# Kernel optimization log

Hardware: AMD Instinct MI355X
Metric: run time of the kernel (lower is better)

The kernel has to match this reference:

```python
import jax, jax.numpy as jnp
import numpy as np

N_NODES = 20000
N_EDGES = 640000
NODE_NF = 64
HIDDEN = 256
N_LAYERS = 4


def _linear_init(key, fan_in, fan_out, layers=None):
    shape = (fan_in, fan_out) if layers is None else (layers, fan_in, fan_out)
    scale = 1.0 / np.sqrt(fan_in)
    return jax.random.normal(key, shape, dtype=jnp.float32) * scale


def setup_inputs() -> dict:
    key = jax.random.key(0)
    ks = jax.random.split(key, 16)
    L, H = N_LAYERS, HIDDEN
    return {
        "h": jax.random.normal(ks[0], (N_NODES, NODE_NF), dtype=jnp.float32),
        "edge_index": jax.random.randint(ks[1], (2, N_EDGES), 0, N_NODES, dtype=jnp.int64),
        "coord_diff": jax.random.normal(ks[2], (N_EDGES, 3), dtype=jnp.float32),
        # embedding in / out
        "w_in": _linear_init(ks[3], NODE_NF, H),
        "b_in": jnp.zeros((H,), jnp.float32),
        "w_out": _linear_init(ks[4], H, NODE_NF),
        "b_out": jnp.zeros((NODE_NF,), jnp.float32),
        # per-layer edge MLP: Linear(2H+1 -> H), silu, Linear(H -> H), silu
        "edge_w1": _linear_init(ks[5], 2 * H + 1, H, L),
        "edge_b1": jnp.zeros((L, H), jnp.float32),
        "edge_w2": _linear_init(ks[6], H, H, L),
        "edge_b2": jnp.zeros((L, H), jnp.float32),
        # per-layer node MLP: Linear(2H -> H), silu, Linear(H -> H)
        "node_w1": _linear_init(ks[7], 2 * H, H, L),
        "node_b1": jnp.zeros((L, H), jnp.float32),
        "node_w2": _linear_init(ks[8], H, H, L),
        "node_b2": jnp.zeros((L, H), jnp.float32),
    }


def reference(h, edge_index, coord_diff, w_in, b_in, w_out, b_out,
              edge_w1, edge_b1, edge_w2, edge_b2,
              node_w1, node_b1, node_w2, node_b2):
    row, col = edge_index[0], edge_index[1]
    # radial is layer-independent: [E, 1]
    radial = jnp.sum(coord_diff ** 2, axis=1, keepdims=True)

    h = h @ w_in + b_in  # [N, H]
    n_nodes = h.shape[0]

    for l in range(N_LAYERS):
        # edge model: gather endpoints, concat with radial, 2-layer MLP
        m = jnp.concatenate([h[row], h[col], radial], axis=1)  # [E, 2H+1]
        m = jax.nn.silu(m @ edge_w1[l] + edge_b1[l])
        m = jax.nn.silu(m @ edge_w2[l] + edge_b2[l])  # [E, H]
        # node model: segment-sum aggregate over row, concat, 2-layer MLP
        agg = jax.ops.segment_sum(m, row, num_segments=n_nodes)  # [N, H]
        x = jnp.concatenate([h, agg], axis=1)  # [N, 2H]
        x = jax.nn.silu(x @ node_w1[l] + node_b1[l])
        h = x @ node_w2[l] + node_b2[l]  # recurrent=False: no residual

    return h @ w_out + b_out  # [N, node_nf]
```

## Files before the change

### kernel.cpp

```cpp
#include <hip/hip_runtime.h>
#include <hip/hip_bf16.h>
#include <cstdint>
#include <cstddef>

#define NN 20000
#define NE 640000
#define NF 64
#define HD 256
#define NL 4
#define HTS 640

typedef __attribute__((ext_vector_type(8))) short short8;
typedef __attribute__((ext_vector_type(4))) float f32x4;
typedef __attribute__((ext_vector_type(2))) float f32x2;

__device__ __forceinline__ float bf2f(unsigned short u){
  union { unsigned int i; float f; } x; x.i = ((unsigned int)u) << 16; return x.f;
}
__device__ __forceinline__ unsigned short f2bf(float f){
  union { float f; unsigned int i; } x; x.f = f;
  unsigned int r = x.i + 0x7FFFu + ((x.i >> 16) & 1u);
  return (unsigned short)(r >> 16);
}
__device__ __forceinline__ unsigned int pk2bf(float a, float b){
  union { __hip_bfloat162 h; unsigned int u; } cv;
  cv.h = __float22bfloat162_rn(float2{a, b});
  return cv.u;
}
__device__ __forceinline__ float silu_f(float v){
  float e = __builtin_amdgcn_exp2f(v * -1.442695041f);
  return v * __builtin_amdgcn_rcpf(1.0f + e);
}
__device__ __forceinline__ f32x2 silu2(f32x2 v){
  f32x2 t = v * (f32x2){-1.442695041f, -1.442695041f};
  f32x2 e = (f32x2){__builtin_amdgcn_exp2f(t.x), __builtin_amdgcn_exp2f(t.y)};
  f32x2 d = e + (f32x2){1.0f, 1.0f};
  f32x2 r = (f32x2){__builtin_amdgcn_rcpf(d.x), __builtin_amdgcn_rcpf(d.y)};
  return v * r;
}
__device__ __forceinline__ void async16(const void* g, void* l){
  __builtin_amdgcn_global_load_lds(
      (const __attribute__((address_space(1))) unsigned int*)g,
      (__attribute__((address_space(3))) unsigned int*)l, 16, 0, 0);
}

__global__ __launch_bounds__(256) void prep_small(
    const float* __restrict__ w_in, const float* __restrict__ w_out,
    const float* __restrict__ ew1, const float* __restrict__ ew2,
    const float* __restrict__ nw1, const float* __restrict__ nw2,
    const float* __restrict__ eb1,
    unsigned short* __restrict__ w_in_t, unsigned short* __restrict__ w_out_t,
    unsigned short* __restrict__ ew1cat, float* __restrict__ w1r,
    float* __restrict__ b1e,
    unsigned short* __restrict__ ew2t, unsigned short* __restrict__ nw1t,
    unsigned short* __restrict__ nw2t)
{
  const int s = blockIdx.y;
  const int tid = blockIdx.x * 256 + threadIdx.x;
  if (s == 18) {
    if (tid < NL * 512) {
      int l = tid >> 9, c = tid & 511;
      b1e[tid] = (c < 256) ? eb1[l * HD + c] : 0.0f;
    }
    return;
  }
  if (s >= 2 && s < 6) {
    int l = s - 2;
    if (tid >= 513 * HD) return;
    int k = tid / HD, n = tid - k * HD;
    float v = ew1[(size_t)l * 513 * HD + tid];
    if (k == 512) { w1r[l * HD + n] = v; return; }
    unsigned short* dst = ew1cat + (size_t)l * 512 * 256;
    if (k < 256) dst[(size_t)n * 256 + k] = f2bf(v);
    else         dst[(size_t)(256 + n) * 256 + (k - 256)] = f2bf(v);
    return;
  }
  const float* src; unsigned short* dst; int K, N;
  if (s == 0)      { src = w_in;  dst = w_in_t;  K = NF;   N = HD; }
  else if (s == 1) { src = w_out; dst = w_out_t; K = HD;   N = NF; }
  else if (s < 10) { int l = s-6;  src = ew2 + (size_t)l*HD*HD;   dst = ew2t + (size_t)l*HD*HD;  K = HD;   N = HD; }
  else if (s < 14) { int l = s-10; src = nw1 + (size_t)l*2*HD*HD; dst = nw1t + (size_t)l*HD*512; K = 2*HD; N = HD; }
  else             { int l = s-14; src = nw2 + (size_t)l*HD*HD;   dst = nw2t + (size_t)l*HD*HD;  K = HD;   N = HD; }
  if (tid >= K * N) return;
  int k = tid / N, n = tid - k * N;
  dst[(size_t)n * K + k] = f2bf(src[tid]);
}

__global__ __launch_bounds__(256) void prep_big(
    const float* __restrict__ h_in, const float* __restrict__ cd,
    unsigned short* __restrict__ hb_in, float* __restrict__ radial)
{
  const int s = blockIdx.y;
  const int tid = blockIdx.x * 256 + threadIdx.x;
  if (s == 0) {
    if (tid < NN * NF) hb_in[tid] = f2bf(h_in[tid]);
  } else {
    if (tid < NE) {
      float x = cd[tid*3+0], y = cd[tid*3+1], z = cd[tid*3+2];
      radial[tid] = x*x + y*y + z*z;
    }
  }
}

__global__ __launch_bounds__(256) void hist_k(const int* __restrict__ erow, int* __restrict__ hist){
  int e = blockIdx.x * 256 + threadIdx.x;
  if (e < NE){
    unsigned r = (unsigned)erow[e]; if (r >= NN) r = 0;
    atomicAdd(&hist[r], 1);
  }
}

__global__ __launch_bounds__(256) void scan_k(const int* __restrict__ hist,
                                              int* __restrict__ starts, int* __restrict__ cursor){
  __shared__ int part[256];
  const int t = threadIdx.x;
  const int CH = 79;
  int lo = t * CH, hi = lo + CH; if (hi > NN) hi = NN; if (lo > NN) lo = NN;
  int s = 0;
  for (int i = lo; i < hi; ++i) s += hist[i];
  part[t] = s; __syncthreads();
  for (int off = 1; off < 256; off <<= 1){
    int v = (t >= off) ? part[t - off] : 0;
    __syncthreads();
    part[t] += v;
    __syncthreads();
  }
  int base = (t == 0) ? 0 : part[t - 1];
  for (int i = lo; i < hi; ++i){ starts[i] = base; cursor[i] = base; base += hist[i]; }
  if (t == 255) starts[NN] = part[255];
}

__global__ __launch_bounds__(256) void scatter_k(const int* __restrict__ erow,
                                                 const int* __restrict__ ecol,
                                                 const float* __restrict__ radial,
                                                 int* __restrict__ cursor,
                                                 int* __restrict__ rowcol,
                                                 float* __restrict__ radial_s){
  int e = blockIdx.x * 256 + threadIdx.x;
  if (e < NE){
    unsigned r = (unsigned)erow[e]; if (r >= NN) r = 0;
    unsigned c = (unsigned)ecol[e]; if (c >= NN) c = 0;
    int pos = atomicAdd(&cursor[r], 1);
    rowcol[2*pos]   = (int)r;
    rowcol[2*pos+1] = (int)c;
    radial_s[pos] = radial[e];
  }
}

__global__ __launch_bounds__(256) void gemm_k(
    const unsigned short* __restrict__ Am, const unsigned short* __restrict__ Wt,
    const float* __restrict__ bias,
    unsigned short* __restrict__ outB, float* __restrict__ outF,
    int M, int N, int K, int lda, int ldc, int fuseSilu)
{
  __shared__ __align__(16) unsigned short As[128*32];
  __shared__ __align__(16) unsigned short Bs[128*32];
  const int t = threadIdx.x;
  const int lane = t & 63, wave = t >> 6;
  const int ln15 = lane & 15, q = lane >> 4;
  const int bm = blockIdx.x, bn = blockIdx.y;
  const int wm = wave >> 1, wn = wave & 1;

  f32x4 acc[4][4];
  #pragma unroll
  for (int i = 0; i < 4; ++i)
    #pragma unroll
    for (int j = 0; j < 4; ++j) acc[i][j] = (f32x4){0.f,0.f,0.f,0.f};

  const int sr = t >> 2;
  const int sc = (t & 3) * 8;
  int am0 = bm*128 + sr;      if (am0 > M-1) am0 = M-1;
  int am1 = bm*128 + 64 + sr; if (am1 > M-1) am1 = M-1;
  int an0 = bn*128 + sr;      if (an0 > N-1) an0 = N-1;
  int an1 = bn*128 + 64 + sr; if (an1 > N-1) an1 = N-1;
  const unsigned short* a0 = Am + (size_t)am0 * lda + sc;
  const unsigned short* a1 = Am + (size_t)am1 * lda + sc;
  const unsigned short* b0 = Wt + (size_t)an0 * K + sc;
  const unsigned short* b1 = Wt + (size_t)an1 * K + sc;

  const int nkt = K >> 5;
  for (int kt = 0; kt < nkt; ++kt) {
    const int k0 = kt * 32;
    async16(a0 + k0, &As[t*8]);
    async16(a1 + k0, &As[2048 + t*8]);
    async16(b0 + k0, &Bs[t*8]);
    async16(b1 + k0, &Bs[2048 + t*8]);
    __syncthreads();
    short8 fa[4], fb[4];
    #pragma unroll
    for (int i = 0; i < 4; ++i)
      fa[i] = *(const short8*)&As[(wm*64 + i*16 + ln15)*32 + q*8];
    #pragma unroll
    for (int j = 0; j < 4; ++j)
      fb[j] = *(const short8*)&Bs[(wn*64 + j*16 + ln15)*32 + q*8];
    #pragma unroll
    for (int i = 0; i < 4; ++i)
      #pragma unroll
      for (int j = 0; j < 4; ++j)
        acc[i][j] = __builtin_amdgcn_mfma_f32_16x16x32_bf16(fa[i], fb[j], acc[i][j], 0, 0, 0);
    __syncthreads();
  }

  #pragma unroll
  for (int i = 0; i < 4; ++i) {
    #pragma unroll
    for (int j = 0; j < 4; ++j) {
      const int n = bn*128 + wn*64 + j*16 + ln15;
      if (n >= N) continue;
      const float bv = bias ? bias[n] : 0.0f;
      #pragma unroll
      for (int r = 0; r < 4; ++r) {
        const int m = bm*128 + wm*64 + i*16 + q*4 + r;
        if (m >= M) continue;
        float v = acc[i][j][r] + bv;
        if (fuseSilu) v = silu_f(v);
        if (outB) outB[(size_t)m * ldc + n] = f2bf(v);
        else      outF[(size_t)m * ldc + n] = v;
      }
    }
  }
}

__global__ __launch_bounds__(256, 4) void node_k(
    unsigned short* __restrict__ hcur,
    float* __restrict__ aggF,
    const unsigned short* __restrict__ w1t,
    const float* __restrict__ b1,
    const unsigned short* __restrict__ w2t,
    const float* __restrict__ b2,
    const unsigned short* __restrict__ w1cat_next,
    const float* __restrict__ b1e_next,
    unsigned short* __restrict__ hT,
    int M)
{
  __shared__ __align__(16) unsigned short As[32*32];
  __shared__ __align__(16) unsigned short Bs[256*32];
  __shared__ __align__(16) unsigned short xL[8*32*32];
  const int t = threadIdx.x;
  const int lane = t & 63, wave = t >> 6;
  const int ln15 = lane & 15, q = lane >> 4;
  const int bm = blockIdx.x;
  const int sc = (t & 3) * 8;
  const int srA = (t & 127) >> 2;
  const int srB = t >> 2;

  const int rowA = bm*32 + srA;
  const unsigned short* aSrc = hcur + (size_t)rowA * HD + sc;
  float* gSrc = aggF + (size_t)rowA * HD + sc;

  float bv1[4], bv2[4];
  #pragma unroll
  for (int j = 0; j < 4; ++j) {
    bv1[j] = b1[wave*64 + j*16 + ln15];
    bv2[j] = b2[wave*64 + j*16 + ln15];
  }

  f32x4 acc[2][4];
  #pragma unroll
  for (int i = 0; i < 2; ++i)
    #pragma unroll
    for (int j = 0; j < 4; ++j) acc[i][j] = (f32x4){0.f,0.f,0.f,0.f};

  for (int kt = 0; kt < 16; ++kt) {
    if (t < 128) {
      if (kt < 8) {
        async16(aSrc + kt*32, &As[t*8]);
      } else {
        float* p = gSrc + (kt-8)*32;
        float4 a0 = *(const float4*)p;
        float4 a1 = *(const float4*)(p + 4);
        union { unsigned int u[4]; short8 s8; } cv;
        cv.u[0] = pk2bf(a0.x, a0.y); cv.u[1] = pk2bf(a0.z, a0.w);
        cv.u[2] = pk2bf(a1.x, a1.y); cv.u[3] = pk2bf(a1.z, a1.w);
        *(float4*)p = float4{0.f,0.f,0.f,0.f};
        *(float4*)(p + 4) = float4{0.f,0.f,0.f,0.f};
        *(short8*)&As[t*8] = cv.s8;
      }
    }
    #pragma unroll
    for (int i = 0; i < 4; ++i)
      async16(w1t + (size_t)(i*64 + srB) * 512 + kt*32 + sc, &Bs[i*2048 + t*8]);
    __syncthreads();
    short8 fa[2], fb[4];
    #pragma unroll
    for (int i = 0; i < 2; ++i) fa[i] = *(const short8*)&As[(i*16 + ln15)*32 + q*8];
    #pragma unroll
    for (int j = 0; j < 4; ++j) fb[j] = *(const short8*)&Bs[(wave*64 + j*16 + ln15)*32 + q*8];
    #pragma unroll
    for (int i = 0; i < 2; ++i)
      #pragma unroll
      for (int j = 0; j < 4; ++j)
        acc[i][j] = __builtin_amdgcn_mfma_f32_16x16x32_bf16(fa[i], fb[j], acc[i][j], 0, 0, 0);
    __syncthreads();
  }

  #pragma unroll
  for (int i = 0; i < 2; ++i) {
    #pragma unroll
    for (int j = 0; j < 4; ++j) {
      const int k = wave*64 + j*16 + ln15;
      const int kt2 = k >> 5, k31 = k & 31;
      const f32x2 bb = (f32x2){bv1[j], bv1[j]};
      f32x2 s01 = (f32x2){acc[i][j][0], acc[i][j][1]} + bb;
      f32x2 s23 = (f32x2){acc[i][j][2], acc[i][j][3]} + bb;
      f32x2 r01 = silu2(s01);
      f32x2 r23 = silu2(s23);
      const int r0 = i*16 + q*4;
      xL[kt2*1024 + (r0  )*32 + k31] = f2bf(r01.x);
      xL[kt2*1024 + (r0+1)*32 + k31] = f2bf(r01.y);
      xL[kt2*1024 + (r0+2)*32 + k31] = f2bf(r23.x);
      xL[kt2*1024 + (r0+3)*32 + k31] = f2bf(r23.y);
    }
  }
  #pragma unroll
  for (int i = 0; i < 2; ++i)
    #pragma unroll
    for (int j = 0; j < 4; ++j) acc[i][j] = (f32x4){0.f,0.f,0.f,0.f};

  for (int kt2 = 0; kt2 < 8; ++kt2) {
    #pragma unroll
    for (int i = 0; i < 4; ++i)
      async16(w2t + (size_t)(i*64 + srB) * 256 + kt2*32 + sc, &Bs[i*2048 + t*8]);
    __syncthreads();
    short8 fa[2], fb[4];
    #pragma unroll
    for (int i = 0; i < 2; ++i) fa[i] = *(const short8*)&xL[kt2*1024 + (i*16 + ln15)*32 + q*8];
    #pragma unroll
    for (int j = 0; j < 4; ++j) fb[j] = *(const short8*)&Bs[(wave*64 + j*16 + ln15)*32 + q*8];
    #pragma unroll
    for (int i = 0; i < 2; ++i)
      #pragma unroll
      for (int j = 0; j < 4; ++j)
        acc[i][j] = __builtin_amdgcn_mfma_f32_16x16x32_bf16(fa[i], fb[j], acc[i][j], 0, 0, 0);
    __syncthreads();
  }

  #pragma unroll
  for (int i = 0; i < 2; ++i) {
    #pragma unroll
    for (int j = 0; j < 4; ++j) {
      const int n = wave*64 + j*16 + ln15;
      const int kt2 = n >> 5, k31 = n & 31;
      float v0 = acc[i][j][0] + bv2[j];
      float v1 = acc[i][j][1] + bv2[j];
      float v2 = acc[i][j][2] + bv2[j];
      float v3 = acc[i][j][3] + bv2[j];
      unsigned short h0 = f2bf(v0), h1 = f2bf(v1), h2 = f2bf(v2), h3 = f2bf(v3);
      const int r0 = i*16 + q*4;
      const int m0 = bm*32 + r0;
      hcur[(size_t)(m0  ) * HD + n] = h0;
      hcur[(size_t)(m0+1) * HD + n] = h1;
      hcur[(size_t)(m0+2) * HD + n] = h2;
      hcur[(size_t)(m0+3) * HD + n] = h3;
      if (w1cat_next) {
        xL[kt2*1024 + (r0  )*32 + k31] = h0;
        xL[kt2*1024 + (r0+1)*32 + k31] = h1;
        xL[kt2*1024 + (r0+2)*32 + k31] = h2;
        xL[kt2*1024 + (r0+3)*32 + k31] = h3;
      }
    }
  }

  if (!w1cat_next) return;

  #pragma unroll
  for (int half = 0; half < 2; ++half) {
    #pragma unroll
    for (int i = 0; i < 2; ++i)
      #pragma unroll
      for (int j = 0; j < 4; ++j) acc[i][j] = (f32x4){0.f,0.f,0.f,0.f};
    for (int kt2 = 0; kt2 < 8; ++kt2) {
      #pragma unroll
      for (int i = 0; i < 4; ++i)
        async16(w1cat_next + (size_t)(half*256 + i*64 + srB) * 256 + kt2*32 + sc,
                &Bs[i*2048 + t*8]);
      __syncthreads();
      short8 fa[2], fb[4];
      #pragma unroll
      for (int i = 0; i < 2; ++i) fa[i] = *(const short8*)&xL[kt2*1024 + (i*16 + ln15)*32 + q*8];
      #pragma unroll
      for (int j = 0; j < 4; ++j) fb[j] = *(const short8*)&Bs[(wave*64 + j*16 + ln15)*32 + q*8];
      #pragma unroll
      for (int i = 0; i < 2; ++i)
        #pragma unroll
        for (int j = 0; j < 4; ++j)
          acc[i][j] = __builtin_amdgcn_mfma_f32_16x16x32_bf16(fa[i], fb[j], acc[i][j], 0, 0, 0);
      __syncthreads();
    }
    #pragma unroll
    for (int i = 0; i < 2; ++i) {
      #pragma unroll
      for (int j = 0; j < 4; ++j) {
        const int n = half*256 + wave*64 + j*16 + ln15;
        const float bv = b1e_next[n];
        #pragma unroll
        for (int r = 0; r < 4; ++r) {
          const int m = bm*32 + i*16 + q*4 + r;
          hT[(size_t)m * HTS + n] = f2bf(acc[i][j][r] + bv);
        }
      }
    }
  }
}

__global__ __launch_bounds__(256, 3) void edge_k(
    const unsigned short* __restrict__ hT,
    const int* __restrict__ rowcol,
    const float* __restrict__ radial_s,
    const float* __restrict__ w1r,
    const unsigned short* __restrict__ w2t,
    const float* __restrict__ b2,
    float* __restrict__ agg)
{
  __shared__ __align__(16) unsigned short MBUF[16896];
  __shared__ int   rowS[64];
  __shared__ float w1rS[256];
  unsigned short* M1  = MBUF;
  unsigned short* m2T = MBUF;

  const int t = threadIdx.x;
  const int lane = t & 63, wave = t >> 6;
  const int ln15 = lane & 15, q = lane >> 4;
  int blk = blockIdx.x;
  blk = (blk & 7) * ((int)gridDim.x >> 3) + (blk >> 3);
  const int e0 = blk * 64;
  const int sr = t >> 2;
  const int sc_swz = (((t & 3) ^ ((sr >> 1) & 3))) * 8;
  const int xq = ((q ^ ((ln15 >> 1) & 3))) * 8;

  const int2 rc = *(const int2*)(rowcol + 2*(e0 + sr));
  int rowv = 0;
  if (t < 64) rowv = rowcol[2*(e0 + t)];
  const float w1v = w1r[t];
  const float rad = radial_s[e0 + sr];

  float bv2[4];
  #pragma unroll
  for (int j = 0; j < 4; ++j) bv2[j] = b2[wave*64 + j*16 + ln15];

  const unsigned short* hr = hT + (size_t)rc.x * HTS + sc_swz;
  const unsigned short* hc = hT + (size_t)rc.y * HTS + 256 + sc_swz;

  short8 va[8], vb[8];
  #pragma unroll
  for (int ch = 0; ch < 8; ++ch) {
    va[ch] = *(const short8*)(hr + ch*32);
    vb[ch] = *(const short8*)(hc + ch*32);
  }

  if (t < 64) rowS[t] = rowv;
  w1rS[t] = w1v;

  const unsigned short* w2row[4];
  #pragma unroll
  for (int j = 0; j < 4; ++j)
    w2row[j] = w2t + (size_t)(wave*64 + j*16 + ln15) * HD + q*8;

  __syncthreads();

  const f32x2 rad2 = (f32x2){rad, rad};
  #pragma unroll
  for (int ch = 0; ch < 8; ++ch) {
    const int c0 = ch*32 + sc_swz;
    const unsigned int* ua = (const unsigned int*)&va[ch];
    const unsigned int* ub = (const unsigned int*)&vb[ch];
    union { unsigned int u[4]; short8 s; } res;
    #pragma unroll
    for (int i = 0; i < 4; ++i) {
      union { unsigned int i; float f; } alo, ahi, blo, bhi;
      alo.i = ua[i] << 16; ahi.i = ua[i] & 0xFFFF0000u;
      blo.i = ub[i] << 16; bhi.i = ub[i] & 0xFFFF0000u;
      f32x2 av = (f32x2){alo.f, ahi.f};
      f32x2 bv = (f32x2){blo.f, bhi.f};
      f32x2 wv = *(const f32x2*)&w1rS[c0 + 2*i];
      f32x2 o = av + bv;
      o = o + rad2 * wv;
      f32x2 sv = silu2(o);
      res.u[i] = pk2bf(sv.x, sv.y);
    }
    *(short8*)&M1[ch*2048 + sr*32 + (t & 3)*8] = res.s;
  }
  __syncthreads();

  f32x4 acc2[4][4];
  #pragma unroll
  for (int i = 0; i < 4; ++i)
    #pragma unroll
    for (int j = 0; j < 4; ++j) acc2[i][j] = (f32x4){0.f,0.f,0.f,0.f};

  __builtin_amdgcn_s_setprio(1);
  #pragma unroll
  for (int kt = 0; kt < 8; ++kt) {
    short8 fa[4], fb[4];
    #pragma unroll
    for (int j = 0; j < 4; ++j) fb[j] = *(const short8*)(w2row[j] + kt*32);
    #pragma unroll
    for (int i = 0; i < 4; ++i) fa[i] = *(const short8*)&M1[kt*2048 + (i*16 + ln15)*32 + xq];
    #pragma unroll
    for (int i = 0; i < 4; ++i)
      #pragma unroll
      for (int j = 0; j < 4; ++j)
        acc2[i][j] = __builtin_amdgcn_mfma_f32_16x16x32_bf16(fa[i], fb[j], acc2[i][j], 0, 0, 0);
  }
  __builtin_amdgcn_s_setprio(0);
  __syncthreads();

  #pragma unroll
  for (int i = 0; i < 4; ++i) {
    #pragma unroll
    for (int j = 0; j < 4; ++j) {
      const int n = wave*64 + j*16 + ln15;
      const f32x2 b2v = (f32x2){bv2[j], bv2[j]};
      f32x2 s01 = (f32x2){acc2[i][j][0], acc2[i][j][1]} + b2v;
      f32x2 s23 = (f32x2){acc2[i][j][2], acc2[i][j][3]} + b2v;
      f32x2 r01 = silu2(s01);
      f32x2 r23 = silu2(s23);
      const int m = i*16 + q*4;
      *(unsigned int*)&m2T[n*66 + m]     = pk2bf(r01.x, r01.y);
      *(unsigned int*)&m2T[n*66 + m + 2] = pk2bf(r23.x, r23.y);
    }
  }
  __syncthreads();

  {
    const int c = t;
    int cur = __builtin_amdgcn_readfirstlane(rowS[0]);
    float s = 0.f;
    #pragma unroll
    for (int m = 0; m < 64; m += 4) {
      unsigned int u0 = *(const unsigned int*)&m2T[c*66 + m];
      unsigned int u1 = *(const unsigned int*)&m2T[c*66 + m + 2];
      int n0 = __builtin_amdgcn_readfirstlane(rowS[m]);
      int n1 = __builtin_amdgcn_readfirstlane(rowS[m+1]);
      int n2 = __builtin_amdgcn_readfirstlane(rowS[m+2]);
      int n3 = __builtin_amdgcn_readfirstlane(rowS[m+3]);
      float f0 = bf2f((unsigned short)u0), f1 = bf2f((unsigned short)(u0 >> 16));
      float f2v = bf2f((unsigned short)u1), f3 = bf2f((unsigned short)(u1 >> 16));
      if (n0 != cur) { atomicAdd(&agg[(size_t)cur * HD + c], s); s = 0.f; cur = n0; }
      s += f0;
      if (n1 != cur) { atomicAdd(&agg[(size_t)cur * HD + c], s); s = 0.f; cur = n1; }
      s += f1;
      if (n2 != cur) { atomicAdd(&agg[(size_t)cur * HD + c], s); s = 0.f; cur = n2; }
      s += f2v;
      if (n3 != cur) { atomicAdd(&agg[(size_t)cur * HD + c], s); s = 0.f; cur = n3; }
      s += f3;
    }
    atomicAdd(&agg[(size_t)cur * HD + c], s);
  }
}

extern "C" void kernel_launch(void* const* d_in, const int* in_sizes, int n_in,
                              void* d_out, int out_size, void* d_ws, size_t ws_size,
                              hipStream_t stream)
{
  (void)in_sizes; (void)n_in; (void)out_size; (void)ws_size;
  const float* h_in  = (const float*)d_in[0];
  const int*   ei    = (const int*)d_in[1];
  const float* cd    = (const float*)d_in[2];
  const float* w_in  = (const float*)d_in[3];
  const float* b_in  = (const float*)d_in[4];
  const float* w_out = (const float*)d_in[5];
  const float* b_out = (const float*)d_in[6];
  const float* ew1   = (const float*)d_in[7];
  const float* eb1   = (const float*)d_in[8];
  const float* ew2   = (const float*)d_in[9];
  const float* eb2   = (const float*)d_in[10];
  const float* nw1   = (const float*)d_in[11];
  const float* nb1   = (const float*)d_in[12];
  const float* nw2   = (const float*)d_in[13];
  const float* nb2   = (const float*)d_in[14];
  float* out = (float*)d_out;

  char* base = (char*)d_ws;
  size_t off = 0;
  auto WS = [&](size_t bytes) -> char* {
    char* p = base + off;
    off = (off + bytes + 255) & ~(size_t)255;
    return p;
  };
  float*          radial  = (float*)WS((size_t)NE * 4);
  unsigned short* hb_in   = (unsigned short*)WS((size_t)NN * NF * 2);
  unsigned short* hcur    = (unsigned short*)WS((size_t)NN * HD * 2);
  float*          aggF    = (float*)WS((size_t)NN * HD * 4);
  unsigned short* hT      = (unsigned short*)WS((size_t)NN * HTS * 2);
  unsigned short* w_in_t  = (unsigned short*)WS((size_t)NF * HD * 2);
  unsigned short* w_out_t = (unsigned short*)WS((size_t)NF * HD * 2);
  unsigned short* ew1cat  = (unsigned short*)WS((size_t)NL * 512 * 256 * 2);
  float*          w1r     = (float*)WS((size_t)NL * HD * 4);
  float*          b1e     = (float*)WS((size_t)NL * 512 * 4);
  unsigned short* ew2t    = (unsigned short*)WS((size_t)NL * HD * HD * 2);
  unsigned short* nw1t    = (unsigned short*)WS((size_t)NL * HD * 512 * 2);
  unsigned short* nw2t    = (unsigned short*)WS((size_t)NL * HD * HD * 2);
  int*            hist    = (int*)WS((size_t)NN * 4);
  int*            starts  = (int*)WS((size_t)(NN + 1) * 4);
  int*            cursor  = (int*)WS((size_t)NN * 4);
  int*            rowcol  = (int*)WS((size_t)NE * 2 * 4);
  float*          radial_s= (float*)WS((size_t)NE * 4);

  hipMemsetAsync(hist, 0, (size_t)NN * 4, stream);
  hipMemsetAsync(aggF, 0, (size_t)NN * HD * 4, stream);
  prep_small<<<dim3(513, 19), 256, 0, stream>>>(w_in, w_out, ew1, ew2, nw1, nw2, eb1,
      w_in_t, w_out_t, ew1cat, w1r, b1e, ew2t, nw1t, nw2t);
  prep_big<<<dim3(5000, 2), 256, 0, stream>>>(h_in, cd, hb_in, radial);
  hist_k<<<NE / 256, 256, 0, stream>>>(ei, hist);
  scan_k<<<1, 256, 0, stream>>>(hist, starts, cursor);
  scatter_k<<<NE / 256, 256, 0, stream>>>(ei, ei + NE, radial, cursor, rowcol, radial_s);

  gemm_k<<<dim3(157, 2), 256, 0, stream>>>(hb_in, w_in_t, b_in, hcur, nullptr,
      NN, HD, NF, NF, HD, 0);
  gemm_k<<<dim3(157, 4), 256, 0, stream>>>(hcur, ew1cat, b1e, hT, nullptr,
      NN, 512, HD, HD, HTS, 0);

  for (int l = 0; l < NL; ++l) {
    edge_k<<<NE / 64, 256, 0, stream>>>(hT, rowcol, radial_s,
        w1r + l * HD, ew2t + (size_t)l * HD * HD, eb2 + l * HD, aggF);
    const int last = (l == NL - 1);
    node_k<<<(NN + 31) / 32, 256, 0, stream>>>(hcur, aggF,
        nw1t + (size_t)l * HD * 512, nb1 + l * HD,
        nw2t + (size_t)l * HD * HD, nb2 + l * HD,
        last ? nullptr : (ew1cat + (size_t)(l+1) * 512 * 256),
        last ? nullptr : (b1e + (size_t)(l+1) * 512),
        hT, NN);
  }

  gemm_k<<<dim3(157, 1), 256, 0, stream>>>(hcur, w_out_t, b_out, nullptr, out,
      NN, NF, HD, HD, NF, 0);
}
```

Measured before the change: 1.224 ms.

## Fuse input embedding and output projection into node kernels, drop generic GEMM

Replaces the two initial GEMM launches (input embedding, then layer-0 edge-W1 projection) with one fused node0_k kernel that keeps the embedded rows in LDS and immediately projects them. The final output projection is folded into the last node_k call, so the last hidden state is consumed from LDS rather than reloaded by a separate GEMM. Edge kernel launch bounds go from 3 to 4 waves per SIMD occupancy hint. This removes launches and global round trips of hcur, at the cost of smaller 32-row tiles and possible register pressure in edge_k.

```diff
diff --git a/kernel.cpp b/kernel.cpp
--- a/kernel.cpp
+++ b/kernel.cpp
@@ -147,54 +147,50 @@
   }
 }
 
-__global__ __launch_bounds__(256) void gemm_k(
-    const unsigned short* __restrict__ Am, const unsigned short* __restrict__ Wt,
-    const float* __restrict__ bias,
-    unsigned short* __restrict__ outB, float* __restrict__ outF,
-    int M, int N, int K, int lda, int ldc, int fuseSilu)
+__global__ __launch_bounds__(256, 4) void node0_k(
+    const unsigned short* __restrict__ hb,
+    const unsigned short* __restrict__ w_in_t,
+    const float* __restrict__ b_in,
+    const unsigned short* __restrict__ w1cat0,
+    const float* __restrict__ b1e0,
+    unsigned short* __restrict__ hcur,
+    unsigned short* __restrict__ hT,
+    int M)
 {
-  __shared__ __align__(16) unsigned short As[128*32];
-  __shared__ __align__(16) unsigned short Bs[128*32];
+  __shared__ __align__(16) unsigned short As[32*64];
+  __shared__ __align__(16) unsigned short Bs[256*32];
+  __shared__ __align__(16) unsigned short xL[8*32*32];
   const int t = threadIdx.x;
   const int lane = t & 63, wave = t >> 6;
   const int ln15 = lane & 15, q = lane >> 4;
-  const int bm = blockIdx.x, bn = blockIdx.y;
-  const int wm = wave >> 1, wn = wave & 1;
-
-  f32x4 acc[4][4];
-  #pragma unroll
-  for (int i = 0; i < 4; ++i)
+  const int bm = blockIdx.x;
+  const int sc = (t & 3) * 8;
+  const int srB = t >> 2;
+
+  float bvin[4];
+  #pragma unroll
+  for (int j = 0; j < 4; ++j) bvin[j] = b_in[wave*64 + j*16 + ln15];
+
+  f32x4 acc[2][4];
+  #pragma unroll
+  for (int i = 0; i < 2; ++i)
     #pragma unroll
     for (int j = 0; j < 4; ++j) acc[i][j] = (f32x4){0.f,0.f,0.f,0.f};
 
-  const int sr = t >> 2;
-  const int sc = (t & 3) * 8;
-  int am0 = bm*128 + sr;      if (am0 > M-1) am0 = M-1;
-  int am1 = bm*128 + 64 + sr; if (am1 > M-1) am1 = M-1;
-  int an0 = bn*128 + sr;      if (an0 > N-1) an0 = N-1;
-  int an1 = bn*128 + 64 + sr; if (an1 > N-1) an1 = N-1;
-  const unsigned short* a0 = Am + (size_t)am0 * lda + sc;
-  const unsigned short* a1 = Am + (size_t)am1 * lda + sc;
-  const unsigned short* b0 = Wt + (size_t)an0 * K + sc;
-  const unsigned short* b1 = Wt + (size_t)an1 * K + sc;
-
-  const int nkt = K >> 5;
-  for (int kt = 0; kt < nkt; ++kt) {
-    const int k0 = kt * 32;
-    async16(a0 + k0, &As[t*8]);
-    async16(a1 + k0, &As[2048 + t*8]);
-    async16(b0 + k0, &Bs[t*8]);
-    async16(b1 + k0, &Bs[2048 + t*8]);
-    __syncthreads();
-    short8 fa[4], fb[4];
+  async16(hb + (size_t)(bm*32 + (t >> 3)) * NF + (t & 7)*8, &As[t*8]);
+
+  for (int kt = 0; kt < 2; ++kt) {
     #pragma unroll
     for (int i = 0; i < 4; ++i)
-      fa[i] = *(const short8*)&As[(wm*64 + i*16 + ln15)*32 + q*8];
-    #pragma unroll
-    for (int j = 0; j < 4; ++j)
-      fb[j] = *(const short8*)&Bs[(wn*64 + j*16 + ln15)*32 + q*8];
-    #pragma unroll
-    for (int i = 0; i < 4; ++i)
+      async16(w_in_t + (size_t)(i*64 + srB) * NF + kt*32 + sc, &Bs[i*2048 + t*8]);
+    __syncthreads();
+    short8 fa[2], fb[4];
+    #pragma unroll
+    for (int i = 0; i < 2; ++i) fa[i] = *(const short8*)&As[(i*16 + ln15)*64 + kt*32 + q*8];
+    #pragma unroll
+    for (int j = 0; j < 4; ++j) fb[j] = *(const short8*)&Bs[(wave*64 + j*16 + ln15)*32 + q*8];
+    #pragma unroll
+    for (int i = 0; i < 2; ++i)
       #pragma unroll
       for (int j = 0; j < 4; ++j)
         acc[i][j] = __builtin_amdgcn_mfma_f32_16x16x32_bf16(fa[i], fb[j], acc[i][j], 0, 0, 0);
@@ -202,23 +198,61 @@
   }
 
   #pragma unroll
-  for (int i = 0; i < 4; ++i) {
+  for (int i = 0; i < 2; ++i) {
     #pragma unroll
     for (int j = 0; j < 4; ++j) {
-      const int n = bn*128 + wn*64 + j*16 + ln15;
-      if (n >= N) continue;
-      const float bv = bias ? bias[n] : 0.0f;
+      const int n = wave*64 + j*16 + ln15;
+      const int kt2 = n >> 5, k31 = n & 31;
+      const int r0 = i*16 + q*4;
+      const int m0 = bm*32 + r0;
       #pragma unroll
       for (int r = 0; r < 4; ++r) {
-        const int m = bm*128 + wm*64 + i*16 + q*4 + r;
-        if (m >= M) continue;
-        float v = acc[i][j][r] + bv;
-        if (fuseSilu) v = silu_f(v);
-        if (outB) outB[(size_t)m * ldc + n] = f2bf(v);
-        else      outF[(size_t)m * ldc + n] = v;
+        unsigned short h = f2bf(acc[i][j][r] + bvin[j]);
+        hcur[(size_t)(m0 + r) * HD + n] = h;
+        xL[kt2*1024 + (r0 + r)*32 + k31] = h;
       }
     }
   }
+
+  #pragma unroll
+  for (int half = 0; half < 2; ++half) {
+    #pragma unroll
+    for (int i = 0; i < 2; ++i)
+      #pragma unroll
+      for (int j = 0; j < 4; ++j) acc[i][j] = (f32x4){0.f,0.f,0.f,0.f};
+    for (int kt2 = 0; kt2 < 8; ++kt2) {
+      #pragma unroll
+      for (int i = 0; i < 4; ++i)
+        async16(w1cat0 + (size_t)(half*256 + i*64 + srB) * 256 + kt2*32 + sc,
+                &Bs[i*2048 + t*8]);
+      __syncthreads();
+      short8 fa[2], fb[4];
+      #pragma unroll
+      for (int i = 0; i < 2; ++i) fa[i] = *(const short8*)&xL[kt2*1024 + (i*16 + ln15)*32 + q*8];
+      #pragma unroll
+      for (int j = 0; j < 4; ++j) fb[j] = *(const short8*)&Bs[(wave*64 + j*16 + ln15)*32 + q*8];
+      #pragma unroll
+      for (int i = 0; i < 2; ++i)
+        #pragma unroll
+        for (int j = 0; j < 4; ++j)
+          acc[i][j] = __builtin_amdgcn_mfma_f32_16x16x32_bf16(fa[i], fb[j], acc[i][j], 0, 0, 0);
+      __syncthreads();
+    }
+    #pragma unroll
+    for (int i = 0; i < 2; ++i) {
+      #pragma unroll
+      for (int j = 0; j < 4; ++j) {
+        const int n = half*256 + wave*64 + j*16 + ln15;
+        const float bv = b1e0[n];
+        #pragma unroll
+        for (int r = 0; r < 4; ++r) {
+          const int m = bm*32 + i*16 + q*4 + r;
+          hT[(size_t)m * HTS + n] = f2bf(acc[i][j][r] + bv);
+        }
+      }
+    }
+  }
+  (void)M;
 }
 
 __global__ __launch_bounds__(256, 4) void node_k(
@@ -231,6 +265,9 @@
     const unsigned short* __restrict__ w1cat_next,
     const float* __restrict__ b1e_next,
     unsigned short* __restrict__ hT,
+    const unsigned short* __restrict__ w_out_t,
+    const float* __restrict__ b_out,
+    float* __restrict__ outF,
     int M)
 {
   __shared__ __align__(16) unsigned short As[32*32];
@@ -341,69 +378,87 @@
     for (int j = 0; j < 4; ++j) {
       const int n = wave*64 + j*16 + ln15;
       const int kt2 = n >> 5, k31 = n & 31;
-      float v0 = acc[i][j][0] + bv2[j];
-      float v1 = acc[i][j][1] + bv2[j];
-      float v2 = acc[i][j][2] + bv2[j];
-      float v3 = acc[i][j][3] + bv2[j];
-      unsigned short h0 = f2bf(v0), h1 = f2bf(v1), h2 = f2bf(v2), h3 = f2bf(v3);
       const int r0 = i*16 + q*4;
       const int m0 = bm*32 + r0;
-      hcur[(size_t)(m0  ) * HD + n] = h0;
-      hcur[(size_t)(m0+1) * HD + n] = h1;
-      hcur[(size_t)(m0+2) * HD + n] = h2;
-      hcur[(size_t)(m0+3) * HD + n] = h3;
-      if (w1cat_next) {
-        xL[kt2*1024 + (r0  )*32 + k31] = h0;
-        xL[kt2*1024 + (r0+1)*32 + k31] = h1;
-        xL[kt2*1024 + (r0+2)*32 + k31] = h2;
-        xL[kt2*1024 + (r0+3)*32 + k31] = h3;
+      #pragma unroll
+      for (int r = 0; r < 4; ++r) {
+        unsigned short h = f2bf(acc[i][j][r] + bv2[j]);
+        hcur[(size_t)(m0 + r) * HD + n] = h;
+        xL[kt2*1024 + (r0 + r)*32 + k31] = h;
       }
     }
   }
 
-  if (!w1cat_next) return;
-
-  #pragma unroll
-  for (int half = 0; half < 2; ++half) {
-    #pragma unroll
-    for (int i = 0; i < 2; ++i)
-      #pragma unroll
-      for (int j = 0; j < 4; ++j) acc[i][j] = (f32x4){0.f,0.f,0.f,0.f};
-    for (int kt2 = 0; kt2 < 8; ++kt2) {
-      #pragma unroll
-      for (int i = 0; i < 4; ++i)
-        async16(w1cat_next + (size_t)(half*256 + i*64 + srB) * 256 + kt2*32 + sc,
-                &Bs[i*2048 + t*8]);
-      __syncthreads();
-      short8 fa[2], fb[4];
-      #pragma unroll
-      for (int i = 0; i < 2; ++i) fa[i] = *(const short8*)&xL[kt2*1024 + (i*16 + ln15)*32 + q*8];
-      #pragma unroll
-      for (int j = 0; j < 4; ++j) fb[j] = *(const short8*)&Bs[(wave*64 + j*16 + ln15)*32 + q*8];
+  if (w1cat_next) {
+    #pragma unroll
+    for (int half = 0; half < 2; ++half) {
       #pragma unroll
       for (int i = 0; i < 2; ++i)
         #pragma unroll
-        for (int j = 0; j < 4; ++j)
-          acc[i][j] = __builtin_amdgcn_mfma_f32_16x16x32_bf16(fa[i], fb[j], acc[i][j], 0, 0, 0);
-      __syncthreads();
-    }
-    #pragma unroll
-    for (int i = 0; i < 2; ++i) {
-      #pragma unroll
-      for (int j = 0; j < 4; ++j) {
-        const int n = half*256 + wave*64 + j*16 + ln15;
-        const float bv = b1e_next[n];
-        #pragma unroll
-        for (int r = 0; r < 4; ++r) {
-          const int m = bm*32 + i*16 + q*4 + r;
-          hT[(size_t)m * HTS + n] = f2bf(acc[i][j][r] + bv);
+        for (int j = 0; j < 4; ++j) acc[i][j] = (f32x4){0.f,0.f,0.f,0.f};
+      for (int kt2 = 0; kt2 < 8; ++kt2) {
+        #pragma unroll
+        for (int i = 0; i < 4; ++i)
+          async16(w1cat_next + (size_t)(half*256 + i*64 + srB) * 256 + kt2*32 + sc,
+                  &Bs[i*2048 + t*8]);
+        __syncthreads();
+        short8 fa[2], fb[4];
+        #pragma unroll
+        for (int i = 0; i < 2; ++i) fa[i] = *(const short8*)&xL[kt2*1024 + (i*16 + ln15)*32 + q*8];
+        #pragma unroll
+        for (int j = 0; j < 4; ++j) fb[j] = *(const short8*)&Bs[(wave*64 + j*16 + ln15)*32 + q*8];
+        #pragma unroll
+        for (int i = 0; i < 2; ++i)
+          #pragma unroll
+          for (int j = 0; j < 4; ++j)
+            acc[i][j] = __builtin_amdgcn_mfma_f32_16x16x32_bf16(fa[i], fb[j], acc[i][j], 0, 0, 0);
+        __syncthreads();
+      }
+      #pragma unroll
+      for (int i = 0; i < 2; ++i) {
+        #pragma unroll
+        for (int j = 0; j < 4; ++j) {
+          const int n = half*256 + wave*64 + j*16 + ln15;
+          const float bv = b1e_next[n];
+          #pragma unroll
+          for (int r = 0; r < 4; ++r) {
+            const int m = bm*32 + i*16 + q*4 + r;
+            hT[(size_t)m * HTS + n] = f2bf(acc[i][j][r] + bv);
+          }
         }
       }
     }
-  }
-}
-
-__global__ __launch_bounds__(256, 3) void edge_k(
+  } else {
+    const int nD = wave*16 + ln15;
+    const float bvD = b_out[nD];
+    f32x4 accD[2];
+    accD[0] = (f32x4){0.f,0.f,0.f,0.f};
+    accD[1] = (f32x4){0.f,0.f,0.f,0.f};
+    for (int kt2 = 0; kt2 < 8; ++kt2) {
+      async16(w_out_t + (size_t)srB * 256 + kt2*32 + sc, &Bs[t*8]);
+      __syncthreads();
+      short8 fa[2], fb;
+      #pragma unroll
+      for (int i = 0; i < 2; ++i) fa[i] = *(const short8*)&xL[kt2*1024 + (i*16 + ln15)*32 + q*8];
+      fb = *(const short8*)&Bs[nD*32 + q*8];
+      #pragma unroll
+      for (int i = 0; i < 2; ++i)
+        accD[i] = __builtin_amdgcn_mfma_f32_16x16x32_bf16(fa[i], fb, accD[i], 0, 0, 0);
+      __syncthreads();
+    }
+    #pragma unroll
+    for (int i = 0; i < 2; ++i) {
+      #pragma unroll
+      for (int r = 0; r < 4; ++r) {
+        const int m = bm*32 + i*16 + q*4 + r;
+        outF[(size_t)m * NF + nD] = accD[i][r] + bvD;
+      }
+    }
+  }
+  (void)M;
+}
+
+__global__ __launch_bounds__(256, 4) void edge_k(
     const unsigned short* __restrict__ hT,
     const int* __restrict__ rowcol,
     const float* __restrict__ radial_s,
@@ -606,23 +661,17 @@
   scan_k<<<1, 256, 0, stream>>>(hist, starts, cursor);
   scatter_k<<<NE / 256, 256, 0, stream>>>(ei, ei + NE, radial, cursor, rowcol, radial_s);
 
-  gemm_k<<<dim3(157, 2), 256, 0, stream>>>(hb_in, w_in_t, b_in, hcur, nullptr,
-      NN, HD, NF, NF, HD, 0);
-  gemm_k<<<dim3(157, 4), 256, 0, stream>>>(hcur, ew1cat, b1e, hT, nullptr,
-      NN, 512, HD, HD, HTS, 0);
+  node0_k<<<NN / 32, 256, 0, stream>>>(hb_in, w_in_t, b_in, ew1cat, b1e, hcur, hT, NN);
 
   for (int l = 0; l < NL; ++l) {
     edge_k<<<NE / 64, 256, 0, stream>>>(hT, rowcol, radial_s,
         w1r + l * HD, ew2t + (size_t)l * HD * HD, eb2 + l * HD, aggF);
     const int last = (l == NL - 1);
-    node_k<<<(NN + 31) / 32, 256, 0, stream>>>(hcur, aggF,
+    node_k<<<NN / 32, 256, 0, stream>>>(hcur, aggF,
         nw1t + (size_t)l * HD * 512, nb1 + l * HD,
         nw2t + (size_t)l * HD * HD, nb2 + l * HD,
         last ? nullptr : (ew1cat + (size_t)(l+1) * 512 * 256),
         last ? nullptr : (b1e + (size_t)(l+1) * 512),
-        hT, NN);
-  }
-
-  gemm_k<<<dim3(157, 1), 256, 0, stream>>>(hcur, w_out_t, b_out, nullptr, out,
-      NN, NF, HD, HD, NF, 0);
-}
+        hT, w_out_t, b_out, out, NN);
+  }
+}
```

Result: faster. 1.146 ms (-6.4%).
